# Performance work log

Hardware: AMD Instinct MI355X
Metric: run time of the kernel (lower is better)

Reference implementation:

```python
import jax, jax.numpy as jnp
import numpy as np


def setup_inputs() -> dict:
    key = jax.random.key(0)
    ks = jax.random.split(key, 8)
    B, L, F, H, A = 128, 196, 2048, 512, 512
    features = jax.random.normal(ks[0], (B, L, F), dtype=jnp.float32)
    hidden_state = jax.random.normal(ks[1], (B, H), dtype=jnp.float32)
    # Linear params (PyTorch layout: weight [out, in], bias [out]); scaled like kaiming-uniform
    W_enc = jax.random.normal(ks[2], (A, F), dtype=jnp.float32) / np.sqrt(F)
    b_enc = jnp.zeros((A,), dtype=jnp.float32)
    W_dec = jax.random.normal(ks[3], (A, H), dtype=jnp.float32) / np.sqrt(H)
    b_dec = jnp.zeros((A,), dtype=jnp.float32)
    W_com = jax.random.normal(ks[4], (1, A), dtype=jnp.float32) / np.sqrt(A)
    b_com = jnp.zeros((1,), dtype=jnp.float32)
    return {
        "features": features, "hidden_state": hidden_state,
        "W_enc": W_enc, "b_enc": b_enc,
        "W_dec": W_dec, "b_dec": b_dec,
        "W_com": W_com, "b_com": b_com,
    }


def reference(features, hidden_state, W_enc, b_enc, W_dec, b_dec, W_com, b_com):
    # encoder_context: [B, L, A]
    enc = jnp.einsum('blf,af->bla', features, W_enc) + b_enc
    # decoder_context: [B, 1, A]
    dec = (hidden_state @ W_dec.T + b_dec)[:, None, :]
    # relu + linear to scalar score (dropout in eval mode = identity): [B, L]
    scores = jnp.einsum('bla,a->bl', jax.nn.relu(enc + dec), W_com[0]) + b_com[0]
    alpha = jax.nn.softmax(scores, axis=1)  # [B, L]
    weighted_features = jnp.einsum('blf,bl->bf', features, alpha)  # [B, F]
    return weighted_features, alpha
```

## Files before the change

kernel.cpp:

```cpp
#include <hip/hip_runtime.h>
#include <hip/hip_bf16.h>
#include <math.h>

#define B_  128
#define L_  196
#define F_  2048
#define H_  512
#define A_  512
#define ML_ (B_*L_)

typedef _Float16 half8 __attribute__((ext_vector_type(8)));
typedef _Float16 half4v __attribute__((ext_vector_type(4)));
typedef _Float16 half2v __attribute__((ext_vector_type(2)));
typedef float f32x4 __attribute__((ext_vector_type(4)));

__device__ __forceinline__ void gld_lds16(const void* g, void* l) {
  __builtin_amdgcn_global_load_lds((const __attribute__((address_space(1))) void*)g,
                                   (__attribute__((address_space(3))) void*)l, 16, 0, 0);
}

__global__ __launch_bounds__(256) void k_prep(const float4* __restrict__ feat4,
                                              half4v* __restrict__ fH,
                                              const float4* __restrict__ Wenc4,
                                              half4v* __restrict__ wH,
                                              const float* __restrict__ hs,
                                              const float* __restrict__ Wdec,
                                              const float* __restrict__ bdec,
                                              const float* __restrict__ benc,
                                              float* __restrict__ dec,
                                              float* __restrict__ scores) {
  __shared__ float h[H_];
  const int bx = blockIdx.x, t = threadIdx.x;

  if (bx < 4096) {
    const int n4 = ML_ * F_ / 4;
    for (int i = bx * 256 + t; i < n4; i += 4096 * 256) {
      const float4 v = feat4[i];
      half4v o = { (_Float16)v.x, (_Float16)v.y, (_Float16)v.z, (_Float16)v.w };
      fH[i] = o;
    }
    return;
  }

  const int b = bx - 4096;
  const int g = b * 256 + t;
  if (g < ML_) scores[g] = 0.f;

  for (int i = b * 256 + t; i < A_ * F_ / 4; i += 128 * 256) {
    const float4 v = Wenc4[i];
    half4v o = { (_Float16)v.x, (_Float16)v.y, (_Float16)v.z, (_Float16)v.w };
    wH[i] = o;
  }

  h[t]       = hs[b * H_ + t];
  h[t + 256] = hs[b * H_ + t + 256];
  __syncthreads();

#pragma unroll
  for (int r = 0; r < 2; r++) {
    const int a = t + r * 256;
    float acc = bdec[a] + benc[a];
    const float4* wr = (const float4*)(Wdec + (size_t)a * H_);
#pragma unroll 4
    for (int k4 = 0; k4 < H_ / 4; k4++) {
      const float4 w = wr[k4];
      acc += w.x * h[4*k4] + w.y * h[4*k4+1] + w.z * h[4*k4+2] + w.w * h[4*k4+3];
    }
    dec[b * A_ + a] = acc;
  }
}

__global__ __launch_bounds__(256) void k_scores_mfma(const _Float16* __restrict__ fA,
                                                     const _Float16* __restrict__ fB,
                                                     const float* __restrict__ dec,
                                                     const float* __restrict__ wcom,
                                                     float* __restrict__ scores) {
  __shared__ _Float16 As[128 * 64];
  __shared__ _Float16 Bs[128 * 64];
  __shared__ float decS[2][128];

  const int tid  = threadIdx.x;
  const int lane = tid & 63;
  const int w    = tid >> 6;
  const int a0   = blockIdx.x * 128;
  const int m0   = blockIdx.y * 128;
  const int wm   = w & 1;
  const int wn   = w >> 1;
  const int quad = lane >> 4;
  const int l16  = lane & 15;

  f32x4 acc[4][4];
#pragma unroll
  for (int i = 0; i < 4; i++)
#pragma unroll
    for (int j = 0; j < 4; j++)
#pragma unroll
      for (int k = 0; k < 4; k++) acc[i][j][k] = 0.f;

  const int b0 = m0 / L_;
  {
    const int i = tid >> 7;
    const int j = tid & 127;
    int bb = b0 + i; if (bb > B_ - 1) bb = B_ - 1;
    decS[i][j] = dec[bb * A_ + a0 + j];
  }

  const int srow   = lane >> 3;
  const int schunk = (lane & 7) ^ srow;
  const _Float16* gAb = fA + (size_t)(m0 + srow) * F_ + schunk * 8;
  const _Float16* gBb = fB + (size_t)(a0 + srow) * F_ + schunk * 8;

  for (int kt = 0; kt < F_; kt += 64) {
#pragma unroll
    for (int i = 0; i < 4; i++) {
      const int r = w * 32 + i * 8;
      gld_lds16(gAb + (size_t)r * F_ + kt, &As[r * 64]);
      gld_lds16(gBb + (size_t)r * F_ + kt, &Bs[r * 64]);
    }
    __syncthreads();

#pragma unroll
    for (int k32 = 0; k32 < 2; k32++) {
      half8 af[4], bf[4];
#pragma unroll
      for (int mt = 0; mt < 4; mt++) {
        const int row = wm * 64 + mt * 16 + l16;
        const int pos = (k32 * 4 + quad) ^ (row & 7);
        af[mt] = *(const half8*)&As[row * 64 + pos * 8];
      }
#pragma unroll
      for (int at = 0; at < 4; at++) {
        const int row = wn * 64 + at * 16 + l16;
        const int pos = (k32 * 4 + quad) ^ (row & 7);
        bf[at] = *(const half8*)&Bs[row * 64 + pos * 8];
      }
#pragma unroll
      for (int mt = 0; mt < 4; mt++)
#pragma unroll
        for (int at = 0; at < 4; at++)
          acc[mt][at] = __builtin_amdgcn_mfma_f32_16x16x32_f16(af[mt], bf[at], acc[mt][at], 0, 0, 0);
    }
    __syncthreads();
  }

  float w4[4];
#pragma unroll
  for (int at = 0; at < 4; at++) w4[at] = wcom[a0 + wn * 64 + at * 16 + l16];

#pragma unroll
  for (int mt = 0; mt < 4; mt++) {
#pragma unroll
    for (int r = 0; r < 4; r++) {
      const int m  = m0 + wm * 64 + mt * 16 + quad * 4 + r;
      const int db = m / L_ - b0;
      float p = 0.f;
#pragma unroll
      for (int at = 0; at < 4; at++) {
        const float e = acc[mt][at][r] + decS[db][wn * 64 + at * 16 + l16];
        p = fmaf(fmaxf(e, 0.f), w4[at], p);
      }
      p += __shfl_xor(p, 1);
      p += __shfl_xor(p, 2);
      p += __shfl_xor(p, 4);
      p += __shfl_xor(p, 8);
      if (l16 == 0) atomicAdd(&scores[m], p);
    }
  }
}

__global__ __launch_bounds__(256) void k_attn(const _Float16* __restrict__ fH,
                                              const float* __restrict__ scores,
                                              float* __restrict__ alpha,
                                              float* __restrict__ out) {
  const int fc = blockIdx.x, b = blockIdx.y, t = threadIdx.x;
  __shared__ float al[L_];
  __shared__ float redm[4];
  __shared__ float reds[4];

  float s = (t < L_) ? scores[b * L_ + t] : -INFINITY;

  float m = s;
#pragma unroll
  for (int o = 32; o >= 1; o >>= 1) m = fmaxf(m, __shfl_xor(m, o));
  if ((t & 63) == 0) redm[t >> 6] = m;
  __syncthreads();
  m = fmaxf(fmaxf(redm[0], redm[1]), fmaxf(redm[2], redm[3]));

  float e = (t < L_) ? expf(s - m) : 0.f;
  float sum = e;
#pragma unroll
  for (int o = 32; o >= 1; o >>= 1) sum += __shfl_xor(sum, o);
  if ((t & 63) == 0) reds[t >> 6] = sum;
  __syncthreads();
  sum = reds[0] + reds[1] + reds[2] + reds[3];

  if (t < L_) {
    const float a = e / sum;
    al[t] = a;
    if (fc == 0) alpha[b * L_ + t] = a;
  }
  __syncthreads();

  const int f0 = fc * 512 + t * 2;
  const half2v* fp = (const half2v*)(fH + (size_t)b * L_ * F_ + f0);
  float ax = 0.f, ay = 0.f;
#pragma unroll 4
  for (int l = 0; l < L_; l++) {
    const half2v v = fp[(size_t)l * (F_ / 2)];
    const float w = al[l];
    ax = fmaf((float)v.x, w, ax);
    ay = fmaf((float)v.y, w, ay);
  }
  float2 o = { ax, ay };
  *(float2*)(out + (size_t)b * F_ + f0) = o;
}

__global__ __launch_bounds__(256) void k_scores(const float* __restrict__ feat,
                                                const float* __restrict__ Wenc,
                                                const float* __restrict__ dec,
                                                const float* __restrict__ wcom,
                                                float* __restrict__ scores) {
  __shared__ float As[16][128];
  __shared__ float Bs[16][128];

  const int tid = threadIdx.x;
  const int m0 = blockIdx.x * 128;
  const int a0 = blockIdx.y * 128;
  const int tx = tid & 15;
  const int ty = tid >> 4;

  float acc[8][8];
#pragma unroll
  for (int i = 0; i < 8; i++)
#pragma unroll
    for (int j = 0; j < 8; j++) acc[i][j] = 0.f;

  for (int kt = 0; kt < F_; kt += 16) {
#pragma unroll
    for (int rep = 0; rep < 2; rep++) {
      const int idx = rep * 256 + tid;
      const int row = idx >> 2;
      const int kp  = (idx & 3) << 2;
      const float4 v = *(const float4*)(feat + (size_t)(m0 + row) * F_ + kt + kp);
      As[kp+0][row] = v.x; As[kp+1][row] = v.y; As[kp+2][row] = v.z; As[kp+3][row] = v.w;
      const float4 w = *(const float4*)(Wenc + (size_t)(a0 + row) * F_ + kt + kp);
      Bs[kp+0][row] = w.x; Bs[kp+1][row] = w.y; Bs[kp+2][row] = w.z; Bs[kp+3][row] = w.w;
    }
    __syncthreads();

#pragma unroll
    for (int k = 0; k < 16; k++) {
      float ar[8], br[8];
      *(float4*)&ar[0] = *(const float4*)&As[k][ty * 8];
      *(float4*)&ar[4] = *(const float4*)&As[k][ty * 8 + 4];
      *(float4*)&br[0] = *(const float4*)&Bs[k][tx * 8];
      *(float4*)&br[4] = *(const float4*)&Bs[k][tx * 8 + 4];
#pragma unroll
      for (int i = 0; i < 8; i++)
#pragma unroll
        for (int j = 0; j < 8; j++) acc[i][j] = fmaf(ar[i], br[j], acc[i][j]);
    }
    __syncthreads();
  }

  float w8[8];
  *(float4*)&w8[0] = *(const float4*)(wcom + a0 + tx * 8);
  *(float4*)&w8[4] = *(const float4*)(wcom + a0 + tx * 8 + 4);

#pragma unroll
  for (int i = 0; i < 8; i++) {
    const int m = m0 + ty * 8 + i;
    const int b = m / L_;
    const float* dp = dec + b * A_ + a0 + tx * 8;
    float p = 0.f;
#pragma unroll
    for (int j = 0; j < 8; j++) {
      const float e = acc[i][j] + dp[j];
      p = fmaf(fmaxf(e, 0.f), w8[j], p);
    }
    p += __shfl_xor(p, 1);
    p += __shfl_xor(p, 2);
    p += __shfl_xor(p, 4);
    p += __shfl_xor(p, 8);
    if (tx == 0) atomicAdd(&scores[m], p);
  }
}

__global__ __launch_bounds__(256) void k_attn_f32(const float* __restrict__ feat,
                                                  const float* __restrict__ scores,
                                                  float* __restrict__ alpha,
                                                  float* __restrict__ out) {
  const int fc = blockIdx.x, b = blockIdx.y, t = threadIdx.x;
  __shared__ float al[L_];
  __shared__ float redm[4];
  __shared__ float reds[4];

  float s = (t < L_) ? scores[b * L_ + t] : -INFINITY;
  float m = s;
#pragma unroll
  for (int o = 32; o >= 1; o >>= 1) m = fmaxf(m, __shfl_xor(m, o));
  if ((t & 63) == 0) redm[t >> 6] = m;
  __syncthreads();
  m = fmaxf(fmaxf(redm[0], redm[1]), fmaxf(redm[2], redm[3]));
  float e = (t < L_) ? expf(s - m) : 0.f;
  float sum = e;
#pragma unroll
  for (int o = 32; o >= 1; o >>= 1) sum += __shfl_xor(sum, o);
  if ((t & 63) == 0) reds[t >> 6] = sum;
  __syncthreads();
  sum = reds[0] + reds[1] + reds[2] + reds[3];
  if (t < L_) {
    const float a = e / sum;
    al[t] = a;
    if (fc == 0) alpha[b * L_ + t] = a;
  }
  __syncthreads();

  const int f0 = fc * 512 + t * 2;
  const float2* fp = (const float2*)(feat + (size_t)b * L_ * F_ + f0);
  float ax = 0.f, ay = 0.f;
#pragma unroll 4
  for (int l = 0; l < L_; l++) {
    const float2 v = fp[(size_t)l * (F_ / 2)];
    const float w = al[l];
    ax = fmaf(v.x, w, ax);
    ay = fmaf(v.y, w, ay);
  }
  float2 o = { ax, ay };
  *(float2*)(out + (size_t)b * F_ + f0) = o;
}

__global__ __launch_bounds__(256) void k_dec_only(const float* __restrict__ hs,
                                                  const float* __restrict__ Wdec,
                                                  const float* __restrict__ bdec,
                                                  const float* __restrict__ benc,
                                                  float* __restrict__ dec,
                                                  float* __restrict__ scores) {
  const int b = blockIdx.x, t = threadIdx.x;
  const int g = b * 256 + t;
  if (g < ML_) scores[g] = 0.f;
  __shared__ float h[H_];
  h[t]       = hs[b * H_ + t];
  h[t + 256] = hs[b * H_ + t + 256];
  __syncthreads();
#pragma unroll
  for (int r = 0; r < 2; r++) {
    const int a = t + r * 256;
    float acc = bdec[a] + benc[a];
    const float4* wr = (const float4*)(Wdec + (size_t)a * H_);
#pragma unroll 4
    for (int k4 = 0; k4 < H_ / 4; k4++) {
      const float4 w = wr[k4];
      acc += w.x * h[4*k4] + w.y * h[4*k4+1] + w.z * h[4*k4+2] + w.w * h[4*k4+3];
    }
    dec[b * A_ + a] = acc;
  }
}

extern "C" void kernel_launch(void* const* d_in, const int* in_sizes, int n_in,
                              void* d_out, int out_size, void* d_ws, size_t ws_size,
                              hipStream_t stream) {
  const float* feat = (const float*)d_in[0];
  const float* hs   = (const float*)d_in[1];
  const float* Wenc = (const float*)d_in[2];
  const float* benc = (const float*)d_in[3];
  const float* Wdec = (const float*)d_in[4];
  const float* bdec = (const float*)d_in[5];
  const float* wcom = (const float*)d_in[6];

  float* out   = (float*)d_out;
  float* alpha = out + B_ * F_;
  float* dec    = (float*)d_ws;
  float* scores = dec + B_ * A_;

  const size_t need = (size_t)(B_ * A_ + ML_) * 4
                    + ((size_t)ML_ * F_ + (size_t)A_ * F_) * 2;

  if (ws_size >= need) {
    _Float16* fH = (_Float16*)(scores + ML_);
    _Float16* wH = fH + (size_t)ML_ * F_;
    k_prep<<<dim3(4096 + 128), dim3(256), 0, stream>>>(
        (const float4*)feat, (half4v*)fH, (const float4*)Wenc, (half4v*)wH,
        hs, Wdec, bdec, benc, dec, scores);
    k_scores_mfma<<<dim3(A_ / 128, ML_ / 128), dim3(256), 0, stream>>>(fH, wH, dec, wcom, scores);
    k_attn<<<dim3(4, B_), dim3(256), 0, stream>>>(fH, scores, alpha, out);
  } else {
    k_dec_only<<<dim3(B_), dim3(256), 0, stream>>>(hs, Wdec, bdec, benc, dec, scores);
    k_scores<<<dim3(ML_ / 128, A_ / 128), dim3(256), 0, stream>>>(feat, Wenc, dec, wcom, scores);
    k_attn_f32<<<dim3(4, B_), dim3(256), 0, stream>>>(feat, scores, alpha, out);
  }
}
```

Baseline: 502.7 us.

## Drop fp16 feature staging; convert fp32 features in LDS inside MFMA GEMM

The full fp16 copy of the features tensor, which cost a large extra read and write pass, is no longer made. The MFMA scores kernel now loads fp32 feature tiles straight into LDS with a new XOR swizzle and converts them to fp16 while building fragments. The attention kernel reads the fp32 features directly. This doubles the LDS footprint and global read bytes for the A operand in the GEMM, and adds conversion work in the inner loop.

```diff
diff --git a/kernel.cpp b/kernel.cpp
--- a/kernel.cpp
+++ b/kernel.cpp
@@ -11,7 +11,6 @@
 
 typedef _Float16 half8 __attribute__((ext_vector_type(8)));
 typedef _Float16 half4v __attribute__((ext_vector_type(4)));
-typedef _Float16 half2v __attribute__((ext_vector_type(2)));
 typedef float f32x4 __attribute__((ext_vector_type(4)));
 
 __device__ __forceinline__ void gld_lds16(const void* g, void* l) {
@@ -19,9 +18,7 @@
                                    (__attribute__((address_space(3))) void*)l, 16, 0, 0);
 }
 
-__global__ __launch_bounds__(256) void k_prep(const float4* __restrict__ feat4,
-                                              half4v* __restrict__ fH,
-                                              const float4* __restrict__ Wenc4,
+__global__ __launch_bounds__(256) void k_prep(const float4* __restrict__ Wenc4,
                                               half4v* __restrict__ wH,
                                               const float* __restrict__ hs,
                                               const float* __restrict__ Wdec,
@@ -29,29 +26,24 @@
                                               const float* __restrict__ benc,
                                               float* __restrict__ dec,
                                               float* __restrict__ scores) {
-  __shared__ float h[H_];
-  const int bx = blockIdx.x, t = threadIdx.x;
-
-  if (bx < 4096) {
-    const int n4 = ML_ * F_ / 4;
-    for (int i = bx * 256 + t; i < n4; i += 4096 * 256) {
-      const float4 v = feat4[i];
-      half4v o = { (_Float16)v.x, (_Float16)v.y, (_Float16)v.z, (_Float16)v.w };
-      fH[i] = o;
-    }
-    return;
-  }
-
-  const int b = bx - 4096;
+  const int b = blockIdx.x, t = threadIdx.x;
+
+  {
+    const int base = b * 2048 + t;
+    float4 v[8];
+#pragma unroll
+    for (int j = 0; j < 8; j++) v[j] = Wenc4[base + j * 256];
+#pragma unroll
+    for (int j = 0; j < 8; j++) {
+      half4v o = { (_Float16)v[j].x, (_Float16)v[j].y, (_Float16)v[j].z, (_Float16)v[j].w };
+      wH[base + j * 256] = o;
+    }
+  }
+
   const int g = b * 256 + t;
   if (g < ML_) scores[g] = 0.f;
 
-  for (int i = b * 256 + t; i < A_ * F_ / 4; i += 128 * 256) {
-    const float4 v = Wenc4[i];
-    half4v o = { (_Float16)v.x, (_Float16)v.y, (_Float16)v.z, (_Float16)v.w };
-    wH[i] = o;
-  }
-
+  __shared__ float h[H_];
   h[t]       = hs[b * H_ + t];
   h[t + 256] = hs[b * H_ + t + 256];
   __syncthreads();
@@ -70,13 +62,13 @@
   }
 }
 
-__global__ __launch_bounds__(256) void k_scores_mfma(const _Float16* __restrict__ fA,
+__global__ __launch_bounds__(256) void k_scores_mfma(const float* __restrict__ fA,
                                                      const _Float16* __restrict__ fB,
                                                      const float* __restrict__ dec,
                                                      const float* __restrict__ wcom,
                                                      float* __restrict__ scores) {
-  __shared__ _Float16 As[128 * 64];
-  __shared__ _Float16 Bs[128 * 64];
+  __shared__ float     As[128 * 64];
+  __shared__ _Float16  Bs[128 * 64];
   __shared__ float decS[2][128];
 
   const int tid  = threadIdx.x;
@@ -105,18 +97,34 @@
     decS[i][j] = dec[bb * A_ + a0 + j];
   }
 
-  const int srow   = lane >> 3;
-  const int schunk = (lane & 7) ^ srow;
-  const _Float16* gAb = fA + (size_t)(m0 + srow) * F_ + schunk * 8;
-  const _Float16* gBb = fB + (size_t)(a0 + srow) * F_ + schunk * 8;
+  const int srow4  = lane >> 4;
+  const int slot16 = lane & 15;
+  const float* pA[8];
+#pragma unroll
+  for (int i = 0; i < 8; i++) {
+    const int rb = w * 32 + i * 4;
+    const int r  = rb + srow4;
+    const int ch = slot16 ^ (r & 15);
+    pA[i] = fA + (size_t)(m0 + r) * F_ + ch * 4;
+  }
+  const int srow8 = lane >> 3;
+  const int slot8 = lane & 7;
+  const _Float16* pB[4];
+#pragma unroll
+  for (int i = 0; i < 4; i++) {
+    const int rb = w * 32 + i * 8;
+    const int r  = rb + srow8;
+    const int ch = slot8 ^ (r & 7);
+    pB[i] = fB + (size_t)(a0 + r) * F_ + ch * 8;
+  }
 
   for (int kt = 0; kt < F_; kt += 64) {
 #pragma unroll
-    for (int i = 0; i < 4; i++) {
-      const int r = w * 32 + i * 8;
-      gld_lds16(gAb + (size_t)r * F_ + kt, &As[r * 64]);
-      gld_lds16(gBb + (size_t)r * F_ + kt, &Bs[r * 64]);
-    }
+    for (int i = 0; i < 8; i++)
+      gld_lds16(pA[i] + kt, &As[(w * 32 + i * 4) * 64]);
+#pragma unroll
+    for (int i = 0; i < 4; i++)
+      gld_lds16(pB[i] + kt, &Bs[(w * 32 + i * 8) * 64]);
     __syncthreads();
 
 #pragma unroll
@@ -125,8 +133,15 @@
 #pragma unroll
       for (int mt = 0; mt < 4; mt++) {
         const int row = wm * 64 + mt * 16 + l16;
-        const int pos = (k32 * 4 + quad) ^ (row & 7);
-        af[mt] = *(const half8*)&As[row * 64 + pos * 8];
+        const int g   = k32 * 8 + quad * 2;
+        const float4 f0 = *(const float4*)&As[row * 64 + ((g    ) ^ l16) * 4];
+        const float4 f1 = *(const float4*)&As[row * 64 + ((g + 1) ^ l16) * 4];
+        half8 a;
+        a[0] = (_Float16)f0.x; a[1] = (_Float16)f0.y;
+        a[2] = (_Float16)f0.z; a[3] = (_Float16)f0.w;
+        a[4] = (_Float16)f1.x; a[5] = (_Float16)f1.y;
+        a[6] = (_Float16)f1.z; a[7] = (_Float16)f1.w;
+        af[mt] = a;
       }
 #pragma unroll
       for (int at = 0; at < 4; at++) {
@@ -168,24 +183,22 @@
   }
 }
 
-__global__ __launch_bounds__(256) void k_attn(const _Float16* __restrict__ fH,
-                                              const float* __restrict__ scores,
-                                              float* __restrict__ alpha,
-                                              float* __restrict__ out) {
+__global__ __launch_bounds__(256) void k_attn_f32(const float* __restrict__ feat,
+                                                  const float* __restrict__ scores,
+                                                  float* __restrict__ alpha,
+                                                  float* __restrict__ out) {
   const int fc = blockIdx.x, b = blockIdx.y, t = threadIdx.x;
   __shared__ float al[L_];
   __shared__ float redm[4];
   __shared__ float reds[4];
 
   float s = (t < L_) ? scores[b * L_ + t] : -INFINITY;
-
   float m = s;
 #pragma unroll
   for (int o = 32; o >= 1; o >>= 1) m = fmaxf(m, __shfl_xor(m, o));
   if ((t & 63) == 0) redm[t >> 6] = m;
   __syncthreads();
   m = fmaxf(fmaxf(redm[0], redm[1]), fmaxf(redm[2], redm[3]));
-
   float e = (t < L_) ? expf(s - m) : 0.f;
   float sum = e;
 #pragma unroll
@@ -193,7 +206,6 @@
   if ((t & 63) == 0) reds[t >> 6] = sum;
   __syncthreads();
   sum = reds[0] + reds[1] + reds[2] + reds[3];
-
   if (t < L_) {
     const float a = e / sum;
     al[t] = a;
@@ -202,39 +214,36 @@
   __syncthreads();
 
   const int f0 = fc * 512 + t * 2;
-  const half2v* fp = (const half2v*)(fH + (size_t)b * L_ * F_ + f0);
+  const float2* fp = (const float2*)(feat + (size_t)b * L_ * F_ + f0);
   float ax = 0.f, ay = 0.f;
 #pragma unroll 4
   for (int l = 0; l < L_; l++) {
-    const half2v v = fp[(size_t)l * (F_ / 2)];
-    const float w = al[l];
-    ax = fmaf((float)v.x, w, ax);
-    ay = fmaf((float)v.y, w, ay);
+    const float2 v = fp[(size_t)l * (F_ / 2)];
+    const float wgt = al[l];
+    ax = fmaf(v.x, wgt, ax);
+    ay = fmaf(v.y, wgt, ay);
   }
   float2 o = { ax, ay };
   *(float2*)(out + (size_t)b * F_ + f0) = o;
 }
 
-__global__ __launch_bounds__(256) void k_scores(const float* __restrict__ feat,
-                                                const float* __restrict__ Wenc,
-                                                const float* __restrict__ dec,
-                                                const float* __restrict__ wcom,
-                                                float* __restrict__ scores) {
+__global__ __launch_bounds__(256) void k_scores_f32(const float* __restrict__ feat,
+                                                    const float* __restrict__ Wenc,
+                                                    const float* __restrict__ dec,
+                                                    const float* __restrict__ wcom,
+                                                    float* __restrict__ scores) {
   __shared__ float As[16][128];
   __shared__ float Bs[16][128];
-
   const int tid = threadIdx.x;
   const int m0 = blockIdx.x * 128;
   const int a0 = blockIdx.y * 128;
   const int tx = tid & 15;
   const int ty = tid >> 4;
-
   float acc[8][8];
 #pragma unroll
   for (int i = 0; i < 8; i++)
 #pragma unroll
     for (int j = 0; j < 8; j++) acc[i][j] = 0.f;
-
   for (int kt = 0; kt < F_; kt += 16) {
 #pragma unroll
     for (int rep = 0; rep < 2; rep++) {
@@ -247,7 +256,6 @@
       Bs[kp+0][row] = w.x; Bs[kp+1][row] = w.y; Bs[kp+2][row] = w.z; Bs[kp+3][row] = w.w;
     }
     __syncthreads();
-
 #pragma unroll
     for (int k = 0; k < 16; k++) {
       float ar[8], br[8];
@@ -262,11 +270,9 @@
     }
     __syncthreads();
   }
-
   float w8[8];
   *(float4*)&w8[0] = *(const float4*)(wcom + a0 + tx * 8);
   *(float4*)&w8[4] = *(const float4*)(wcom + a0 + tx * 8 + 4);
-
 #pragma unroll
   for (int i = 0; i < 8; i++) {
     const int m = m0 + ty * 8 + i;
@@ -284,50 +290,6 @@
     p += __shfl_xor(p, 8);
     if (tx == 0) atomicAdd(&scores[m], p);
   }
-}
-
-__global__ __launch_bounds__(256) void k_attn_f32(const float* __restrict__ feat,
-                                                  const float* __restrict__ scores,
-                                                  float* __restrict__ alpha,
-                                                  float* __restrict__ out) {
-  const int fc = blockIdx.x, b = blockIdx.y, t = threadIdx.x;
-  __shared__ float al[L_];
-  __shared__ float redm[4];
-  __shared__ float reds[4];
-
-  float s = (t < L_) ? scores[b * L_ + t] : -INFINITY;
-  float m = s;
-#pragma unroll
-  for (int o = 32; o >= 1; o >>= 1) m = fmaxf(m, __shfl_xor(m, o));
-  if ((t & 63) == 0) redm[t >> 6] = m;
-  __syncthreads();
-  m = fmaxf(fmaxf(redm[0], redm[1]), fmaxf(redm[2], redm[3]));
-  float e = (t < L_) ? expf(s - m) : 0.f;
-  float sum = e;
-#pragma unroll
-  for (int o = 32; o >= 1; o >>= 1) sum += __shfl_xor(sum, o);
-  if ((t & 63) == 0) reds[t >> 6] = sum;
-  __syncthreads();
-  sum = reds[0] + reds[1] + reds[2] + reds[3];
-  if (t < L_) {
-    const float a = e / sum;
-    al[t] = a;
-    if (fc == 0) alpha[b * L_ + t] = a;
-  }
-  __syncthreads();
-
-  const int f0 = fc * 512 + t * 2;
-  const float2* fp = (const float2*)(feat + (size_t)b * L_ * F_ + f0);
-  float ax = 0.f, ay = 0.f;
-#pragma unroll 4
-  for (int l = 0; l < L_; l++) {
-    const float2 v = fp[(size_t)l * (F_ / 2)];
-    const float w = al[l];
-    ax = fmaf(v.x, w, ax);
-    ay = fmaf(v.y, w, ay);
-  }
-  float2 o = { ax, ay };
-  *(float2*)(out + (size_t)b * F_ + f0) = o;
 }
 
 __global__ __launch_bounds__(256) void k_dec_only(const float* __restrict__ hs,
@@ -373,20 +335,16 @@
   float* dec    = (float*)d_ws;
   float* scores = dec + B_ * A_;
 
-  const size_t need = (size_t)(B_ * A_ + ML_) * 4
-                    + ((size_t)ML_ * F_ + (size_t)A_ * F_) * 2;
+  const size_t need = (size_t)(B_ * A_ + ML_) * 4 + (size_t)A_ * F_ * 2;
 
   if (ws_size >= need) {
-    _Float16* fH = (_Float16*)(scores + ML_);
-    _Float16* wH = fH + (size_t)ML_ * F_;
-    k_prep<<<dim3(4096 + 128), dim3(256), 0, stream>>>(
-        (const float4*)feat, (half4v*)fH, (const float4*)Wenc, (half4v*)wH,
-        hs, Wdec, bdec, benc, dec, scores);
-    k_scores_mfma<<<dim3(A_ / 128, ML_ / 128), dim3(256), 0, stream>>>(fH, wH, dec, wcom, scores);
-    k_attn<<<dim3(4, B_), dim3(256), 0, stream>>>(fH, scores, alpha, out);
+    _Float16* wH = (_Float16*)(scores + ML_);
+    k_prep<<<dim3(128), dim3(256), 0, stream>>>(
+        (const float4*)Wenc, (half4v*)wH, hs, Wdec, bdec, benc, dec, scores);
+    k_scores_mfma<<<dim3(A_ / 128, ML_ / 128), dim3(256), 0, stream>>>(feat, wH, dec, wcom, scores);
   } else {
     k_dec_only<<<dim3(B_), dim3(256), 0, stream>>>(hs, Wdec, bdec, benc, dec, scores);
-    k_scores<<<dim3(ML_ / 128, A_ / 128), dim3(256), 0, stream>>>(feat, Wenc, dec, wcom, scores);
-    k_attn_f32<<<dim3(4, B_), dim3(256), 0, stream>>>(feat, scores, alpha, out);
-  }
-}
+    k_scores_f32<<<dim3(ML_ / 128, A_ / 128), dim3(256), 0, stream>>>(feat, Wenc, dec, wcom, scores);
+  }
+  k_attn_f32<<<dim3(4, B_), dim3(256), 0, stream>>>(feat, scores, alpha, out);
+}
```

After: 500.2 us. About the same (-0.5%).
